# Kernel tuning notes

Measured on AMD Instinct MI355X. Metric: run time of the kernel, lower is better.

## Reference

```python
import jax, jax.numpy as jnp
import numpy as np
from jax import lax

D, NTOK, HEADS, DH, DEPTH, KCODE = 512, 256, 16, 32, 12, 2048

def _ln(x, g, b):
    m = x.mean(-1, keepdims=True)
    v = x.var(-1, keepdims=True)
    return (x - m) / jnp.sqrt(v + 1e-5) * g + b

def _attn(x, g, bln, wqkv, wo, bo):
    b, n, _ = x.shape
    xn = _ln(x, g, bln)
    qkv = xn @ wqkv  # [b,n,3*H*DH]
    q, k, v = jnp.split(qkv, 3, axis=-1)
    def h(t):
        return t.reshape(b, n, HEADS, DH).transpose(0, 2, 1, 3)  # bhnd
    q, k, v = h(q), h(k), h(v)
    dots = jnp.einsum('bhid,bhjd->bhij', q, k) * (DH ** -0.5)
    a = jax.nn.softmax(dots, axis=-1)
    o = jnp.einsum('bhij,bhjd->bhid', a, v).transpose(0, 2, 1, 3).reshape(b, n, HEADS * DH)
    return x + o @ wo + bo

def _conv3(x, w):  # w [out,in,3,3], pad 1
    return lax.conv_general_dilated(x, w, (1, 1), [(1, 1), (1, 1)],
                                    dimension_numbers=('NCHW', 'OIHW', 'NCHW'))

def _convT2(x, w, b):  # torch ConvTranspose2d k=2,s=2; w torch-shape [in,out,2,2]
    wk = jnp.transpose(w, (1, 0, 2, 3))[:, :, ::-1, ::-1]
    y = lax.conv_general_dilated(x, wk, (1, 1), [(1, 1), (1, 1)], lhs_dilation=(2, 2),
                                 dimension_numbers=('NCHW', 'OIHW', 'NCHW'))
    return y + b[None, :, None, None]

def _bn_relu(x, g, b):  # training-mode BatchNorm2d (biased var) + ReLU
    m = x.mean((0, 2, 3), keepdims=True)
    v = x.var((0, 2, 3), keepdims=True)
    xn = (x - m) / jnp.sqrt(v + 1e-5)
    return jax.nn.relu(xn * g[None, :, None, None] + b[None, :, None, None])

def setup_inputs() -> dict:
    key = jax.random.key(0)
    ks = iter(jax.random.split(key, 64))
    r = lambda *s: jax.random.normal(next(ks), s, dtype=jnp.float32)
    w = lambda *s: 0.02 * jax.random.normal(next(ks), s, dtype=jnp.float32)
    inp = {
        'x': r(16, 512, 16, 16),
        'feat0': r(16, 64, 128, 128),
        'feat1': r(16, 128, 64, 64),
        'feat2': r(16, 256, 32, 32),
        'pos_emb': r(1, NTOK, D),
        'codebook': r(KCODE, D),
        'ln_g': jnp.ones((DEPTH, D)), 'ln_b': jnp.zeros((DEPTH, D)),
        'wqkv': w(DEPTH, D, 3 * HEADS * DH),
        'wo': w(DEPTH, HEADS * DH, D), 'bo': jnp.zeros((DEPTH, D)),
        'up_w0': w(512, 256, 2, 2), 'up_b0': jnp.zeros((256,)),
        'cw0a': w(256, 512, 3, 3), 'g0a': jnp.ones((256,)), 'b0a': jnp.zeros((256,)),
        'cw0b': w(256, 256, 3, 3), 'g0b': jnp.ones((256,)), 'b0b': jnp.zeros((256,)),
        'up_w1': w(256, 128, 2, 2), 'up_b1': jnp.zeros((128,)),
        'cw1a': w(128, 256, 3, 3), 'g1a': jnp.ones((128,)), 'b1a': jnp.zeros((128,)),
        'cw1b': w(128, 128, 3, 3), 'g1b': jnp.ones((128,)), 'b1b': jnp.zeros((128,)),
        'up_w2': w(128, 64, 2, 2), 'up_b2': jnp.zeros((64,)),
        'cw2a': w(64, 128, 3, 3), 'g2a': jnp.ones((64,)), 'b2a': jnp.zeros((64,)),
        'cw2b': w(64, 64, 3, 3), 'g2b': jnp.ones((64,)), 'b2b': jnp.zeros((64,)),
        'last_w': w(1, 64, 1, 1), 'last_b': jnp.zeros((1,)),
    }
    return inp

def reference(x, feat0, feat1, feat2, pos_emb, codebook, ln_g, ln_b, wqkv, wo, bo,
              up_w0, up_b0, cw0a, g0a, b0a, cw0b, g0b, b0b,
              up_w1, up_b1, cw1a, g1a, b1a, cw1b, g1b, b1b,
              up_w2, up_b2, cw2a, g2a, b2a, cw2b, g2b, b2b,
              last_w, last_b):
    b = x.shape[0]
    # ViT encoder: flatten spatial -> tokens, add pos embedding, 12 residual attn layers
    tok = x.reshape(b, D, NTOK).transpose(0, 2, 1) + pos_emb  # [b,256,512]
    for i in range(DEPTH):
        tok = _attn(tok, ln_g[i], ln_b[i], wqkv[i], wo[i], bo[i])
    # VQ codebook quantization: squared-euclidean argmin + gather + straight-through
    flat = tok.reshape(-1, D)
    d2 = (flat * flat).sum(-1, keepdims=True) - 2.0 * flat @ codebook.T + (codebook * codebook).sum(-1)
    idx = jnp.argmin(d2, axis=-1)
    q = codebook[idx].reshape(b, NTOK, D)
    quant = tok + lax.stop_gradient(q - tok)
    y = quant.transpose(0, 2, 1).reshape(b, D, 16, 16)
    # conv decoder with skip connections (DecoderCup blocks)
    y = _convT2(y, up_w0, up_b0)                      # [b,256,32,32]
    y = jnp.concatenate([y, feat2], axis=1)           # [b,512,32,32]
    y = _bn_relu(_conv3(y, cw0a), g0a, b0a)
    y = _bn_relu(_conv3(y, cw0b), g0b, b0b)
    y = _convT2(y, up_w1, up_b1)                      # [b,128,64,64]
    y = jnp.concatenate([y, feat1], axis=1)
    y = _bn_relu(_conv3(y, cw1a), g1a, b1a)
    y = _bn_relu(_conv3(y, cw1b), g1b, b1b)
    y = _convT2(y, up_w2, up_b2)                      # [b,64,128,128]
    y = jnp.concatenate([y, feat0], axis=1)
    y = _bn_relu(_conv3(y, cw2a), g2a, b2a)
    y = _bn_relu(_conv3(y, cw2b), g2b, b2b)
    y = lax.conv_general_dilated(y, last_w, (1, 1), [(0, 0), (0, 0)],
                                 dimension_numbers=('NCHW', 'OIHW', 'NCHW')) + last_b[None, :, None, None]
    return jax.nn.sigmoid(y)  # [b,1,128,128]
```

## Files before the change

kernel.cpp:

```cpp
#include <hip/hip_runtime.h>

#define B_    16
#define NTOK  256
#define D_    512
#define HEADS 16
#define DH    32
#define DEPTH 12
#define KCODE 2048
#define M_    (B_*NTOK)
#define BN_S  512

typedef __attribute__((ext_vector_type(8))) short short8;
typedef __attribute__((ext_vector_type(4))) float float4v;
typedef __attribute__((ext_vector_type(16))) float float16v;
typedef __attribute__((ext_vector_type(4))) unsigned int uint4v;
typedef __attribute__((ext_vector_type(2))) unsigned int uint2v;
typedef unsigned short ushort;

__device__ __forceinline__ ushort f2b(float f){
  union { float f; unsigned u; } v; v.f = f;
  unsigned r = v.u + 0x7FFFu + ((v.u >> 16) & 1u);
  return (ushort)(r >> 16);
}
__device__ __forceinline__ float b2f(ushort h){
  union { unsigned u; float f; } v; v.u = ((unsigned)h) << 16; return v.f;
}
__device__ __forceinline__ float bits2f(unsigned u){
  union { unsigned u; float f; } v; v.u = u; return v.f;
}

typedef __attribute__((address_space(3))) unsigned int lds_uint;
typedef __attribute__((address_space(1))) const unsigned int glob_uint;
__device__ __forceinline__ void gl_lds16(const ushort* g, ushort* l){
  __builtin_amdgcn_global_load_lds((glob_uint*)g, (lds_uint*)l, 16, 0, 0);
}


__global__ void k_tok_init(const float* __restrict__ x, const float* __restrict__ pos,
                           float* __restrict__ tok){
  __shared__ float t[32][33];
  const int t0 = blockIdx.x*32, d0 = blockIdx.y*32, b = blockIdx.z;
  const int tx = threadIdx.x, ty = threadIdx.y;
  #pragma unroll
  for (int i = 0; i < 4; ++i){
    int d = d0 + ty + i*8;
    t[ty + i*8][tx] = x[((size_t)(b*D_ + d))*NTOK + t0 + tx];
  }
  __syncthreads();
  #pragma unroll
  for (int i = 0; i < 4; ++i){
    int tt = t0 + ty + i*8;
    tok[((size_t)(b*NTOK + tt))*D_ + d0 + tx] = t[tx][ty + i*8] + pos[(size_t)tt*D_ + d0 + tx];
  }
}

__global__ void k_split(const float* __restrict__ src, ushort* __restrict__ oh,
                        ushort* __restrict__ ol, int n){
  int i = blockIdx.x*256 + threadIdx.x;
  if (i >= n) return;
  float v = src[i];
  ushort h = f2b(v);
  oh[i] = h; ol[i] = f2b(v - b2f(h));
}

__global__ void k_split_t(const float* __restrict__ src, ushort* __restrict__ oh,
                          ushort* __restrict__ ol, int K, int N){
  __shared__ float t[32][33];
  const int n0 = blockIdx.x*32, k0 = blockIdx.y*32;
  const size_t lb = (size_t)blockIdx.z*K*N;
  const int tx = threadIdx.x, ty = threadIdx.y;
  #pragma unroll
  for (int i = 0; i < 4; ++i){
    int k = k0 + ty + i*8;
    t[ty + i*8][tx] = src[lb + (size_t)k*N + n0 + tx];
  }
  __syncthreads();
  #pragma unroll
  for (int i = 0; i < 4; ++i){
    int n = n0 + ty + i*8;
    float v = t[tx][ty + i*8];
    ushort h = f2b(v);
    size_t o = lb + (size_t)n*K + k0 + tx;
    oh[o] = h; ol[o] = f2b(v - b2f(h));
  }
}

__global__ void k_w9(const float* __restrict__ w, ushort* __restrict__ W9,
                     int Cin, int Cout){
  int i = blockIdx.x*256 + threadIdx.x;
  if (i >= Cout*Cin*9) return;
  int co = i / (Cin*9); int r = i - co*(Cin*9);
  int ci = r / 9; int tap = r - ci*9;
  W9[((size_t)tap*Cout + co)*Cin + ci] = f2b(w[i]);
}

__global__ void k_upw(const float* __restrict__ w, ushort* __restrict__ Wt4,
                      int Cin, int Cout){
  int i = blockIdx.x*256 + threadIdx.x;
  if (i >= Cin*Cout*4) return;
  int ci = i / (Cout*4); int r = i - ci*(Cout*4);
  int co = r >> 2; int tap = r & 3;
  Wt4[((size_t)tap*Cout + co)*Cin + ci] = f2b(w[i]);
}

__global__ __launch_bounds__(256) void k_ln_split(
    const float* __restrict__ in, ushort* __restrict__ oh,
    ushort* __restrict__ ol, const float* __restrict__ g,
    const float* __restrict__ bta){
  const int lane = threadIdx.x & 63;
  const int row  = blockIdx.x*4 + (threadIdx.x >> 6);
  const float* xr = in + (size_t)row*D_ + lane*8;
  float4v v0 = *(const float4v*)xr;
  float4v v1 = *(const float4v*)(xr + 4);
  float s = v0.x+v0.y+v0.z+v0.w + v1.x+v1.y+v1.z+v1.w;
  float q = v0.x*v0.x+v0.y*v0.y+v0.z*v0.z+v0.w*v0.w
          + v1.x*v1.x+v1.y*v1.y+v1.z*v1.z+v1.w*v1.w;
  #pragma unroll
  for (int off = 32; off > 0; off >>= 1){
    s += __shfl_xor(s, off, 64);
    q += __shfl_xor(q, off, 64);
  }
  float mean = s * (1.f/D_);
  float var  = q * (1.f/D_) - mean*mean;
  float inv  = rsqrtf(var + 1e-5f);
  float4v g0 = *(const float4v*)(g + lane*8);
  float4v g1 = *(const float4v*)(g + lane*8 + 4);
  float4v b0 = *(const float4v*)(bta + lane*8);
  float4v b1 = *(const float4v*)(bta + lane*8 + 4);
  float xv[8] = {v0.x,v0.y,v0.z,v0.w,v1.x,v1.y,v1.z,v1.w};
  float gv[8] = {g0.x,g0.y,g0.z,g0.w,g1.x,g1.y,g1.z,g1.w};
  float bv[8] = {b0.x,b0.y,b0.z,b0.w,b1.x,b1.y,b1.z,b1.w};
  unsigned hw[4], lw[4];
  #pragma unroll
  for (int p = 0; p < 4; ++p){
    float ya = (xv[2*p]   - mean)*inv*gv[2*p]   + bv[2*p];
    float yb = (xv[2*p+1] - mean)*inv*gv[2*p+1] + bv[2*p+1];
    ushort ha = f2b(ya), hb = f2b(yb);
    hw[p] = (unsigned)ha | ((unsigned)hb << 16);
    lw[p] = (unsigned)f2b(ya - b2f(ha)) | ((unsigned)f2b(yb - b2f(hb)) << 16);
  }
  size_t o = (size_t)row*D_ + lane*8;
  *(uint4v*)(oh + o) = uint4v{hw[0], hw[1], hw[2], hw[3]};
  *(uint4v*)(ol + o) = uint4v{lw[0], lw[1], lw[2], lw[3]};
}

__global__ __launch_bounds__(256,2) void k_gemm_split(
    const ushort* __restrict__ Ah, const ushort* __restrict__ Al,
    const ushort* __restrict__ Bh, const ushort* __restrict__ Bl,
    float* __restrict__ C, const float* __restrict__ bias,
    const float* __restrict__ resid, int M, int N, int K){
  __shared__ ushort Ash[128][32], Asl[128][32], Bsh[128][32], Bsl[128][32];
  const int tid = threadIdx.x;
  const int m_base = blockIdx.x*128, n_base = blockIdx.y*128;
  const int lane = tid & 63, wv = tid >> 6;
  const int quad = lane >> 4, r16 = lane & 15;
  const int m_off = (wv & 1)*64, n_off = (wv >> 1)*64;
  const int lrow = lane >> 2, lseg = lane & 3;
  const int row0 = wv*32 + lrow;
  const int us   = lseg ^ ((row0 >> 1) & 3);
  const size_t offA0 = (size_t)(m_base + row0)*K + us*8;
  const size_t offA1 = offA0 + (size_t)16*K;
  const size_t offB0 = (size_t)(n_base + row0)*K + us*8;
  const size_t offB1 = offB0 + (size_t)16*K;
  ushort* lAh = &Ash[0][0] + wv*1024;
  ushort* lAl = &Asl[0][0] + wv*1024;
  ushort* lBh = &Bsh[0][0] + wv*1024;
  ushort* lBl = &Bsl[0][0] + wv*1024;
  float4v acc[4][4];
  #pragma unroll
  for (int i = 0; i < 4; ++i)
    #pragma unroll
    for (int j = 0; j < 4; ++j) acc[i][j] = float4v{0.f,0.f,0.f,0.f};
  for (int k0 = 0; k0 < K; k0 += 32){
    gl_lds16(Ah + offA0 + k0, lAh);
    gl_lds16(Ah + offA1 + k0, lAh + 512);
    gl_lds16(Al + offA0 + k0, lAl);
    gl_lds16(Al + offA1 + k0, lAl + 512);
    gl_lds16(Bh + offB0 + k0, lBh);
    gl_lds16(Bh + offB1 + k0, lBh + 512);
    gl_lds16(Bl + offB0 + k0, lBl);
    gl_lds16(Bl + offB1 + k0, lBl + 512);
    __syncthreads();
    short8 ah[4], al[4], bh[4], bl[4];
    #pragma unroll
    for (int i = 0; i < 4; ++i){
      int ra = m_off + i*16 + r16;
      int rb = n_off + i*16 + r16;
      int sa = (quad ^ ((ra >> 1) & 3))*8;
      int sb = (quad ^ ((rb >> 1) & 3))*8;
      ah[i] = *(const short8*)&Ash[ra][sa];
      al[i] = *(const short8*)&Asl[ra][sa];
      bh[i] = *(const short8*)&Bsh[rb][sb];
      bl[i] = *(const short8*)&Bsl[rb][sb];
    }
    #pragma unroll
    for (int i = 0; i < 4; ++i)
      #pragma unroll
      for (int j = 0; j < 4; ++j){
        acc[i][j] = __builtin_amdgcn_mfma_f32_16x16x32_bf16(bh[j], ah[i], acc[i][j], 0,0,0);
        acc[i][j] = __builtin_amdgcn_mfma_f32_16x16x32_bf16(bh[j], al[i], acc[i][j], 0,0,0);
        acc[i][j] = __builtin_amdgcn_mfma_f32_16x16x32_bf16(bl[j], ah[i], acc[i][j], 0,0,0);
      }
    __syncthreads();
  }
  #pragma unroll
  for (int i = 0; i < 4; ++i){
    int m = m_base + m_off + i*16 + r16;
    #pragma unroll
    for (int j = 0; j < 4; ++j){
      int n = n_base + n_off + j*16 + quad*4;
      float4v v = acc[i][j];
      if (bias)  v += *(const float4v*)(bias + n);
      if (resid) v += *(const float4v*)(resid + (size_t)m*N + n);
      *(float4v*)(C + (size_t)m*N + n) = v;
    }
  }
}

__global__ __launch_bounds__(512) void k_attn2(const float* __restrict__ qkv,
                                               ushort* __restrict__ oh,
                                               ushort* __restrict__ ol){
  __shared__ float4v smem[NTOK*16];
  float4v* ks = smem;
  float4v* vs = smem + NTOK*8;
  const int h = blockIdx.x, b = blockIdx.y, t = threadIdx.x;
  const int tq = t & 255, half = t >> 8;
  const float* base = qkv + (size_t)b*NTOK*1536;
  const int koff = 512 + h*DH, voff = 1024 + h*DH;
  for (int i = t; i < NTOK*8; i += 512){
    int j = i >> 3, d4 = i & 7;
    ks[i] = *(const float4v*)(base + (size_t)j*1536 + koff + d4*4);
    vs[i] = *(const float4v*)(base + (size_t)j*1536 + voff + d4*4);
  }
  float4v q8[8];
  const float* qrow = base + (size_t)tq*1536 + h*DH;
  #pragma unroll
  for (int d4 = 0; d4 < 8; ++d4) q8[d4] = *(const float4v*)(qrow + d4*4);
  __syncthreads();
  float4v o8[8];
  #pragma unroll
  for (int d4 = 0; d4 < 8; ++d4) o8[d4] = float4v{0.f,0.f,0.f,0.f};
  float l = 0.f;
  const int j0 = half*128, j1 = j0 + 128;
  for (int j = j0; j < j1; ++j){
    float s = 0.f;
    #pragma unroll
    for (int d4 = 0; d4 < 8; ++d4){
      float4v kk = ks[j*8 + d4];
      s += q8[d4].x*kk.x + q8[d4].y*kk.y + q8[d4].z*kk.z + q8[d4].w*kk.w;
    }
    float e = __expf(s * 0.17677669529663689f);
    l += e;
    #pragma unroll
    for (int d4 = 0; d4 < 8; ++d4){
      float4v vv = vs[j*8 + d4];
      o8[d4].x += e*vv.x; o8[d4].y += e*vv.y; o8[d4].z += e*vv.z; o8[d4].w += e*vv.w;
    }
  }
  __syncthreads();
  if (half){
    float4v* st = smem + (size_t)tq*9;
    #pragma unroll
    for (int d4 = 0; d4 < 8; ++d4) st[d4] = o8[d4];
    ((float*)smem)[9216 + tq] = l;
  }
  __syncthreads();
  if (!half){
    const float4v* st = smem + (size_t)tq*9;
    #pragma unroll
    for (int d4 = 0; d4 < 8; ++d4) o8[d4] += st[d4];
    l += ((float*)smem)[9216 + tq];
    float inv = 1.f / l;
    size_t ob = (size_t)(b*NTOK + tq)*D_ + h*DH;
    #pragma unroll
    for (int d4 = 0; d4 < 8; ++d4){
      float vals[4] = {o8[d4].x*inv, o8[d4].y*inv, o8[d4].z*inv, o8[d4].w*inv};
      #pragma unroll
      for (int r = 0; r < 4; ++r){
        ushort hh = f2b(vals[r]);
        oh[ob + d4*4 + r] = hh;
        ol[ob + d4*4 + r] = f2b(vals[r] - b2f(hh));
      }
    }
  }
}

__global__ void k_cnorm(const float* __restrict__ cb, float* __restrict__ cnorm){
  int k = blockIdx.x, t = threadIdx.x;
  float v1 = cb[(size_t)k*D_ + t];
  float v2 = cb[(size_t)k*D_ + t + 256];
  __shared__ float r[256];
  r[t] = v1*v1 + v2*v2;
  __syncthreads();
  for (int off=128; off>0; off>>=1){
    if (t<off) r[t]+=r[t+off];
    __syncthreads();
  }
  if (t==0) cnorm[k] = r[0];
}

__global__ void k_argmin(const float* __restrict__ d2, const float* __restrict__ cnorm,
                         int* __restrict__ idx){
  int m = blockIdx.x, t = threadIdx.x;
  float best = 3.4e38f; int bk = 0;
  for (int k = t; k < KCODE; k += 256){
    float s = cnorm[k] - 2.f*d2[(size_t)m*KCODE + k];
    if (s < best){ best = s; bk = k; }
  }
  __shared__ float bs[256]; __shared__ int bi[256];
  bs[t]=best; bi[t]=bk;
  __syncthreads();
  for (int off=128; off>0; off>>=1){
    if (t<off){
      if (bs[t+off] < bs[t] || (bs[t+off]==bs[t] && bi[t+off]<bi[t])){
        bs[t]=bs[t+off]; bi[t]=bi[t+off];
      }
    }
    __syncthreads();
  }
  if (t==0) idx[m] = bi[0];
}

__global__ void k_gather_nhwc(const float* __restrict__ cb, const int* __restrict__ idx,
                              ushort* __restrict__ y0){
  int i = blockIdx.x*256 + threadIdx.x;
  if (i >= B_*NTOK*D_) return;
  int d = i % D_; int r = i / D_; int t = r % NTOK; int b = r / NTOK;
  y0[i] = f2b(cb[(size_t)idx[b*NTOK + t]*D_ + d]);
}


__global__ __launch_bounds__(256,2) void k_conv16(
    const ushort* __restrict__ X, const ushort* __restrict__ W9,
    float* __restrict__ Y, int Cin, int Cout, int H, int W){
  __shared__ ushort Xs[324][34];
  __shared__ ushort Ws[576][34];
  const int HW = H*W;
  const int tid = threadIdx.x;
  const int b = blockIdx.z;
  const int tiles_w = W >> 4;
  const int th0 = (blockIdx.x / tiles_w) * 16;
  const int tw0 = (blockIdx.x - (blockIdx.x / tiles_w)*tiles_w) * 16;
  const int n_base = blockIdx.y*64;
  const int lane = tid & 63, wv = tid >> 6;
  const int l31 = lane & 31, hi8 = (lane >> 5)*8;
  const ushort* Xb = X + (size_t)b*HW*Cin;
  const ushort* sptr[6]; ushort* sdst[6]; bool sok[6];
  #pragma unroll
  for (int e = 0; e < 6; ++e){
    int item = tid + e*256;
    int row = item >> 2;
    int seg = item & 3;
    if (row > 323) row = 323;
    int ph = row / 18, pw = row - ph*18;
    int gh = th0 + ph - 1, gw = tw0 + pw - 1;
    bool ok = gh >= 0 && gh < H && gw >= 0 && gw < W;
    int pidx = ok ? (gh*W + gw) : 0;
    sok[e] = ok;
    sptr[e] = Xb + ((size_t)pidx*Cin + seg*8);
    sdst[e] = &Xs[row][seg*8];
  }
  const ushort* wptr[9]; ushort* wdst[9];
  #pragma unroll
  for (int e = 0; e < 9; ++e){
    int item = tid + e*256;
    int row = item >> 2;
    int seg = item & 3;
    int tap = row >> 6, co = row & 63;
    wdst[e] = &Ws[row][seg*8];
    wptr[e] = W9 + ((size_t)tap*Cout + n_base + co)*Cin + seg*8;
  }
  const uint4v zz = {};
  float16v a00={}, a01={}, a10={}, a11={};
  const int lrow = (lane & 15) + ((lane & 16) ? 18 : 0);
  const int pr0 = wv*72 + lrow;
  for (int k0 = 0; k0 < Cin; k0 += 32){
    if (k0) __syncthreads();
    #pragma unroll
    for (int e = 0; e < 6; ++e){
      if (e < 5 || tid < 16){
        uint4v v = sok[e] ? *(const uint4v*)(sptr[e] + k0) : zz;
        *(uint4v*)sdst[e] = v;
      }
    }
    #pragma unroll
    for (int e = 0; e < 9; ++e)
      *(uint4v*)wdst[e] = *(const uint4v*)(wptr[e] + k0);
    __syncthreads();
    #pragma unroll
    for (int s = 0; s < 2; ++s){
      const int kc = s*16 + hi8;
      #pragma unroll
      for (int tap = 0; tap < 9; ++tap){
        const int kh = tap/3, kw = tap - (tap/3)*3;
        const int xr = pr0 + kh*18 + kw;
        short8 x0 = *(const short8*)&Xs[xr     ][kc];
        short8 x1 = *(const short8*)&Xs[xr + 36][kc];
        short8 w0 = *(const short8*)&Ws[tap*64      + l31][kc];
        short8 w1 = *(const short8*)&Ws[tap*64 + 32 + l31][kc];
        a00 = __builtin_amdgcn_mfma_f32_32x32x16_bf16(w0, x0, a00, 0,0,0);
        a01 = __builtin_amdgcn_mfma_f32_32x32x16_bf16(w0, x1, a01, 0,0,0);
        a10 = __builtin_amdgcn_mfma_f32_32x32x16_bf16(w1, x0, a10, 0,0,0);
        a11 = __builtin_amdgcn_mfma_f32_32x32x16_bf16(w1, x1, a11, 0,0,0);
      }
    }
  }
  float* Yb = Y + (size_t)b*HW*Cout;
  const int co4 = (lane >> 5)*4;
  #pragma unroll
  for (int i = 0; i < 2; ++i){
    int p = wv*64 + i*32 + l31;
    int gp = (th0 + (p >> 4))*W + tw0 + (p & 15);
    float* yr = Yb + (size_t)gp*Cout + n_base + co4;
    float16v A0 = i ? a01 : a00;
    float16v A1 = i ? a11 : a10;
    #pragma unroll
    for (int q = 0; q < 4; ++q){
      float4v v0 = {A0[4*q+0], A0[4*q+1], A0[4*q+2], A0[4*q+3]};
      float4v v1 = {A1[4*q+0], A1[4*q+1], A1[4*q+2], A1[4*q+3]};
      *(float4v*)(yr + 8*q)      = v0;
      *(float4v*)(yr + 32 + 8*q) = v1;
    }
  }
}

__global__ __launch_bounds__(256) void k_upconv_nhwc(
    const ushort* __restrict__ X, const ushort* __restrict__ Wt4,
    const float* __restrict__ bias, ushort* __restrict__ CC,
    int Cin, int Cout, int Hi, int Wi, int Ctot){
  __shared__ ushort Xs[64][40], Ws[4][64][40];
  const int HWi = Hi*Wi;
  const int tid = threadIdx.x;
  const int b = blockIdx.z;
  const int m_base = blockIdx.x*64;
  const int n_base = blockIdx.y*64;
  const int lane = tid & 63, wv = tid >> 6;
  const int quad = lane >> 4, r16 = lane & 15;
  const int m_off = (wv & 1)*32, n_off = (wv >> 1)*32;
  const int srow = tid & 63, skq = tid >> 6;
  const ushort* xrow = X + ((size_t)b*HWi + m_base + srow)*Cin + skq*8;
  const ushort* w0 = Wt4 + ((size_t)0*Cout + n_base + srow)*Cin + skq*8;
  const ushort* w1 = Wt4 + ((size_t)1*Cout + n_base + srow)*Cin + skq*8;
  const ushort* w2 = Wt4 + ((size_t)2*Cout + n_base + srow)*Cin + skq*8;
  const ushort* w3 = Wt4 + ((size_t)3*Cout + n_base + srow)*Cin + skq*8;
  float4v acc[4][4];
  #pragma unroll
  for (int t = 0; t < 4; ++t)
    #pragma unroll
    for (int q = 0; q < 4; ++q) acc[t][q] = float4v{0.f,0.f,0.f,0.f};
  for (int k0 = 0; k0 < Cin; k0 += 32){
    *(uint4v*)&Xs[srow][skq*8]    = *(const uint4v*)(xrow + k0);
    *(uint4v*)&Ws[0][srow][skq*8] = *(const uint4v*)(w0 + k0);
    *(uint4v*)&Ws[1][srow][skq*8] = *(const uint4v*)(w1 + k0);
    *(uint4v*)&Ws[2][srow][skq*8] = *(const uint4v*)(w2 + k0);
    *(uint4v*)&Ws[3][srow][skq*8] = *(const uint4v*)(w3 + k0);
    __syncthreads();
    short8 xf0 = *(const short8*)&Xs[m_off      + r16][quad*8];
    short8 xf1 = *(const short8*)&Xs[m_off + 16 + r16][quad*8];
    #pragma unroll
    for (int t = 0; t < 4; ++t){
      short8 wf0 = *(const short8*)&Ws[t][n_off      + r16][quad*8];
      short8 wf1 = *(const short8*)&Ws[t][n_off + 16 + r16][quad*8];
      acc[t][0] = __builtin_amdgcn_mfma_f32_16x16x32_bf16(wf0, xf0, acc[t][0], 0,0,0);
      acc[t][1] = __builtin_amdgcn_mfma_f32_16x16x32_bf16(wf0, xf1, acc[t][1], 0,0,0);
      acc[t][2] = __builtin_amdgcn_mfma_f32_16x16x32_bf16(wf1, xf0, acc[t][2], 0,0,0);
      acc[t][3] = __builtin_amdgcn_mfma_f32_16x16x32_bf16(wf1, xf1, acc[t][3], 0,0,0);
    }
    __syncthreads();
  }
  const int Wo = 2*Wi, HWo = 4*HWi;
  int co0 = n_base + n_off + quad*4, co1 = co0 + 16;
  float4v bv0 = *(const float4v*)(bias + co0);
  float4v bv1 = *(const float4v*)(bias + co1);
  int px0 = m_base + m_off + r16, px1 = px0 + 16;
  #pragma unroll
  for (int j = 0; j < 2; ++j){
    int p = j ? px1 : px0;
    int r = p / Wi, c = p - r*Wi;
    #pragma unroll
    for (int t = 0; t < 4; ++t){
      int opix = (2*r + (t>>1))*Wo + 2*c + (t&1);
      ushort* o = CC + ((size_t)b*HWo + opix)*Ctot;
      float4v vA = acc[t][0 + j] + bv0;
      float4v vB = acc[t][2 + j] + bv1;
      uint2v pA, pB;
      pA.x = (unsigned)f2b(vA.x) | ((unsigned)f2b(vA.y) << 16);
      pA.y = (unsigned)f2b(vA.z) | ((unsigned)f2b(vA.w) << 16);
      pB.x = (unsigned)f2b(vB.x) | ((unsigned)f2b(vB.y) << 16);
      pB.y = (unsigned)f2b(vB.z) | ((unsigned)f2b(vB.w) << 16);
      *(uint2v*)(o + co0) = pA;
      *(uint2v*)(o + co1) = pB;
    }
  }
}

__global__ void k_feat2cc(const float* __restrict__ feat, ushort* __restrict__ cc,
                          int Cf, int Coff, int Ctot, int HW){
  __shared__ ushort t[32][33];
  int pb = blockIdx.x*32, cbs = blockIdx.y*32, b = blockIdx.z;
  int tx = threadIdx.x, ty = threadIdx.y;
  #pragma unroll
  for (int i = 0; i < 4; ++i){
    int c = cbs + ty + i*8;
    t[ty + i*8][tx] = f2b(feat[((size_t)(b*Cf) + c)*HW + pb + tx]);
  }
  __syncthreads();
  #pragma unroll
  for (int i = 0; i < 4; ++i){
    int p = pb + ty + i*8;
    cc[((size_t)b*HW + p)*Ctot + Coff + cbs + tx] = t[tx][ty + i*8];
  }
}

__global__ __launch_bounds__(256) void k_bnstats_nhwc(
    const float* __restrict__ x, float* __restrict__ part, int C, int HW){
  const int s = blockIdx.x, tid = threadIdx.x;
  const int R = B_*HW;
  const int chunk = R / BN_S;
  const int L = C >> 2;
  const int G = 256 / L;
  const int c4 = tid % L, g = tid / L;
  float4v a = {}, q = {};
  const float* xb = x + (size_t)(s*chunk)*C + 4*c4;
  for (int r = g; r < chunk; r += G){
    float4v v = *(const float4v*)(xb + (size_t)r*C);
    a += v; q += v*v;
  }
  __shared__ float4v h1[256], h2[256];
  h1[tid] = a; h2[tid] = q;
  __syncthreads();
  if (tid < L){
    float4v ra = h1[tid], rq = h2[tid];
    for (int gg = 1; gg < G; ++gg){ ra += h1[tid + gg*L]; rq += h2[tid + gg*L]; }
    int c0 = 4*c4;
    part[(size_t)(c0+0)*BN_S + s] = ra.x;
    part[(size_t)(c0+1)*BN_S + s] = ra.y;
    part[(size_t)(c0+2)*BN_S + s] = ra.z;
    part[(size_t)(c0+3)*BN_S + s] = ra.w;
    part[(size_t)(C+c0+0)*BN_S + s] = rq.x;
    part[(size_t)(C+c0+1)*BN_S + s] = rq.y;
    part[(size_t)(C+c0+2)*BN_S + s] = rq.z;
    part[(size_t)(C+c0+3)*BN_S + s] = rq.w;
  }
}

__global__ void k_bnfinal(const float* __restrict__ part, const float* __restrict__ g,
                          const float* __restrict__ bb, float* __restrict__ scale,
                          float* __restrict__ shift, int C, int cnt){
  int c = blockIdx.x, t = threadIdx.x;
  __shared__ float r1[256], r2[256];
  r1[t] = part[(size_t)c*BN_S + t]       + part[(size_t)c*BN_S + t + 256];
  r2[t] = part[(size_t)(C + c)*BN_S + t] + part[(size_t)(C + c)*BN_S + t + 256];
  __syncthreads();
  for (int off = 128; off > 0; off >>= 1){
    if (t < off){ r1[t] += r1[t+off]; r2[t] += r2[t+off]; }
    __syncthreads();
  }
  if (t == 0){
    float m = r1[0]/cnt;
    float v = r2[0]/cnt - m*m;
    float sc = g[c]*rsqrtf(v + 1e-5f);
    scale[c] = sc;
    shift[c] = bb[c] - m*sc;
  }
}

__global__ void k_bnapply_nhwc(const float* __restrict__ x, ushort* __restrict__ y,
                               const float* __restrict__ scale,
                               const float* __restrict__ shift, int C, int n4){
  int i = blockIdx.x*256 + threadIdx.x;
  if (i >= n4) return;
  float4v v = *(const float4v*)(x + (size_t)4*i);
  int c0 = (4*i) % C;
  float4v sc = *(const float4v*)(scale + c0);
  float4v sh = *(const float4v*)(shift + c0);
  float r0 = fmaxf(v.x*sc.x + sh.x, 0.f);
  float r1 = fmaxf(v.y*sc.y + sh.y, 0.f);
  float r2 = fmaxf(v.z*sc.z + sh.z, 0.f);
  float r3 = fmaxf(v.w*sc.w + sh.w, 0.f);
  uint2v pk;
  pk.x = (unsigned)f2b(r0) | ((unsigned)f2b(r1) << 16);
  pk.y = (unsigned)f2b(r2) | ((unsigned)f2b(r3) << 16);
  *(uint2v*)(y + (size_t)4*i) = pk;
}

__global__ void k_last_nhwc(const ushort* __restrict__ x, const float* __restrict__ lw,
                            const float* __restrict__ lb, float* __restrict__ out){
  __shared__ float wsm[64];
  int tid = threadIdx.x;
  if (tid < 64) wsm[tid] = lw[tid];
  __syncthreads();
  int i = blockIdx.x*256 + tid;
  const uint4v* xr = (const uint4v*)(x + (size_t)i*64);
  float acc = lb[0];
  #pragma unroll
  for (int q = 0; q < 8; ++q){
    uint4v u = xr[q];
    unsigned uu[4] = {u.x, u.y, u.z, u.w};
    #pragma unroll
    for (int k = 0; k < 4; ++k){
      acc += bits2f(uu[k] << 16)          * wsm[q*8 + 2*k];
      acc += bits2f(uu[k] & 0xffff0000u)  * wsm[q*8 + 2*k + 1];
    }
  }
  out[i] = 1.f/(1.f + __expf(-acc));
}

#define MBx 1048576ull

static inline void run_conv16(const ushort* in, const float* w, ushort* W9,
                              float* out, int Cin, int Cout, int H, int W,
                              hipStream_t stream){
  int total = Cout*Cin*9;
  k_w9<<<(total+255)/256, 256, 0, stream>>>(w, W9, Cin, Cout);
  k_conv16<<<dim3((H>>4)*(W>>4), Cout/64, B_), 256, 0, stream>>>(in, W9, out, Cin, Cout, H, W);
}

static inline void run_bn(const float* x, ushort* y, float* part, float* scale, float* shift,
                          const float* g, const float* bb, int C, int HW, hipStream_t stream){
  k_bnstats_nhwc<<<BN_S, 256, 0, stream>>>(x, part, C, HW);
  k_bnfinal<<<C, 256, 0, stream>>>(part, g, bb, scale, shift, C, B_*HW);
  int n4 = B_*HW*C/4;
  k_bnapply_nhwc<<<(n4+255)/256, 256, 0, stream>>>(x, y, scale, shift, C, n4);
}

extern "C" void kernel_launch(void* const* d_in, const int* in_sizes, int n_in,
                              void* d_out, int out_size, void* d_ws, size_t ws_size,
                              hipStream_t stream){
  const float* x     = (const float*)d_in[0];
  const float* feat0 = (const float*)d_in[1];
  const float* feat1 = (const float*)d_in[2];
  const float* feat2 = (const float*)d_in[3];
  const float* pos   = (const float*)d_in[4];
  const float* cb    = (const float*)d_in[5];
  const float* ln_g  = (const float*)d_in[6];
  const float* ln_b  = (const float*)d_in[7];
  const float* wqkv  = (const float*)d_in[8];
  const float* wo    = (const float*)d_in[9];
  const float* bo    = (const float*)d_in[10];
  const float* up_w0 = (const float*)d_in[11];
  const float* up_b0 = (const float*)d_in[12];
  const float* cw0a  = (const float*)d_in[13];
  const float* g0a   = (const float*)d_in[14];
  const float* b0a   = (const float*)d_in[15];
  const float* cw0b  = (const float*)d_in[16];
  const float* g0b   = (const float*)d_in[17];
  const float* b0b   = (const float*)d_in[18];
  const float* up_w1 = (const float*)d_in[19];
  const float* up_b1 = (const float*)d_in[20];
  const float* cw1a  = (const float*)d_in[21];
  const float* g1a   = (const float*)d_in[22];
  const float* b1a   = (const float*)d_in[23];
  const float* cw1b  = (const float*)d_in[24];
  const float* g1b   = (const float*)d_in[25];
  const float* b1b   = (const float*)d_in[26];
  const float* up_w2 = (const float*)d_in[27];
  const float* up_b2 = (const float*)d_in[28];
  const float* cw2a  = (const float*)d_in[29];
  const float* g2a   = (const float*)d_in[30];
  const float* b2a   = (const float*)d_in[31];
  const float* cw2b  = (const float*)d_in[32];
  const float* g2b   = (const float*)d_in[33];
  const float* b2b   = (const float*)d_in[34];
  const float* lw    = (const float*)d_in[35];
  const float* lb    = (const float*)d_in[36];

  char* ws = (char*)d_ws;
  float*  tok     = (float*) (ws);
  ushort* xn_hi   = (ushort*)(ws +  8388608ull);
  ushort* xn_lo   = (ushort*)(ws + 12582912ull);
  float*  qkv     = (float*) (ws + 16777216ull);
  ushort* at_hi   = (ushort*)(ws + 41943040ull);
  ushort* at_lo   = (ushort*)(ws + 46137344ull);
  ushort* tok_hi  = (ushort*)(ws + 50331648ull);
  ushort* tok_lo  = (ushort*)(ws + 54525952ull);
  ushort* Wq_hi   = (ushort*)(ws + 58720256ull);
  ushort* Wq_lo   = (ushort*)(ws + 77594624ull);
  ushort* Wo_hi   = (ushort*)(ws + 96468992ull);
  ushort* Wo_lo   = (ushort*)(ws + 102760448ull);
  ushort* cb_hi   = (ushort*)(ws + 109051904ull);
  ushort* cb_lo   = (ushort*)(ws + 111149056ull);
  float*  cnorm   = (float*) (ws + 113246208ull);
  int*    idx     = (int*)   (ws + 113254400ull);
  float*  d2      = (float*) (ws + 58720256ull);
  ushort* W9   = (ushort*)(ws + 134*MBx);
  float* bnsc  = (float*) (ws + 136*MBx + 524288);
  float* bnsh  = (float*) (ws + 136*MBx + 528384);
  ushort* Wt4  = (ushort*)(ws + 137*MBx);
  float* bnp   = (float*) (ws + 138*MBx);
  ushort* y0   = (ushort*)(ws + 139*MBx);
  ushort* cc0 = (ushort*)(ws + 146*MBx);
  float*  va0 = (float*) (ws + 163*MBx);
  ushort* xa0 = (ushort*)(ws + 180*MBx);
  float*  vb0 = (float*) (ws + 146*MBx);
  ushort* xb0 = (ushort*)(ws + 189*MBx);
  ushort* cc1 = (ushort*)(ws + 0*MBx);
  float*  va1 = (float*) (ws + 34*MBx);
  ushort* xa1 = (ushort*)(ws + 68*MBx);
  float*  vb1 = (float*) (ws + 85*MBx);
  ushort* xb1 = (ushort*)(ws + 146*MBx);
  ushort* cc2 = (ushort*)(ws + 0*MBx);
  float*  va2 = (float*) (ws + 67*MBx);
  ushort* xa2 = (ushort*)(ws + 146*MBx);
  float*  vb2 = (float*) (ws + 0*MBx);
  ushort* xb2 = (ushort*)(ws + 67*MBx);

  k_split_t<<<dim3(1536/32, D_/32, DEPTH), dim3(32,8), 0, stream>>>(wqkv, Wq_hi, Wq_lo, D_, 1536);
  k_split_t<<<dim3(D_/32, D_/32, DEPTH), dim3(32,8), 0, stream>>>(wo, Wo_hi, Wo_lo, D_, D_);
  k_split<<<(KCODE*D_+255)/256, 256, 0, stream>>>(cb, cb_hi, cb_lo, KCODE*D_);
  k_cnorm<<<KCODE, 256, 0, stream>>>(cb, cnorm);

  k_tok_init<<<dim3(NTOK/32, D_/32, B_), dim3(32,8), 0, stream>>>(x, pos, tok);
  for (int l = 0; l < DEPTH; ++l){
    k_ln_split<<<M_/4, 256, 0, stream>>>(tok, xn_hi, xn_lo, ln_g + l*D_, ln_b + l*D_);
    k_gemm_split<<<dim3(M_/128, 1536/128), 256, 0, stream>>>(
        xn_hi, xn_lo, Wq_hi + (size_t)l*1536*D_, Wq_lo + (size_t)l*1536*D_,
        qkv, nullptr, nullptr, M_, 1536, D_);
    k_attn2<<<dim3(HEADS, B_), 512, 0, stream>>>(qkv, at_hi, at_lo);
    k_gemm_split<<<dim3(M_/128, D_/128), 256, 0, stream>>>(
        at_hi, at_lo, Wo_hi + (size_t)l*D_*D_, Wo_lo + (size_t)l*D_*D_,
        tok, bo + l*D_, tok, M_, D_, D_);
  }

  k_split<<<(M_*D_+255)/256, 256, 0, stream>>>(tok, tok_hi, tok_lo, M_*D_);
  k_gemm_split<<<dim3(M_/128, KCODE/128), 256, 0, stream>>>(
      tok_hi, tok_lo, cb_hi, cb_lo, d2, nullptr, nullptr, M_, KCODE, D_);
  k_argmin<<<M_, 256, 0, stream>>>(d2, cnorm, idx);
  k_gather_nhwc<<<(B_*NTOK*D_)/256, 256, 0, stream>>>(cb, idx, y0);

  k_upw<<<(512*256*4+255)/256, 256, 0, stream>>>(up_w0, Wt4, 512, 256);
  k_upconv_nhwc<<<dim3(256/64, 256/64, B_), 256, 0, stream>>>(y0, Wt4, up_b0, cc0, 512, 256, 16, 16, 512);
  k_feat2cc<<<dim3(1024/32, 256/32, B_), dim3(32,8), 0, stream>>>(feat2, cc0, 256, 256, 512, 1024);
  run_conv16(cc0, cw0a, W9, va0, 512, 256, 32, 32, stream);
  run_bn(va0, xa0, bnp, bnsc, bnsh, g0a, b0a, 256, 1024, stream);
  run_conv16(xa0, cw0b, W9, vb0, 256, 256, 32, 32, stream);
  run_bn(vb0, xb0, bnp, bnsc, bnsh, g0b, b0b, 256, 1024, stream);

  k_upw<<<(256*128*4+255)/256, 256, 0, stream>>>(up_w1, Wt4, 256, 128);
  k_upconv_nhwc<<<dim3(1024/64, 128/64, B_), 256, 0, stream>>>(xb0, Wt4, up_b1, cc1, 256, 128, 32, 32, 256);
  k_feat2cc<<<dim3(4096/32, 128/32, B_), dim3(32,8), 0, stream>>>(feat1, cc1, 128, 128, 256, 4096);
  run_conv16(cc1, cw1a, W9, va1, 256, 128, 64, 64, stream);
  run_bn(va1, xa1, bnp, bnsc, bnsh, g1a, b1a, 128, 4096, stream);
  run_conv16(xa1, cw1b, W9, vb1, 128, 128, 64, 64, stream);
  run_bn(vb1, xb1, bnp, bnsc, bnsh, g1b, b1b, 128, 4096, stream);

  k_upw<<<(128*64*4+255)/256, 256, 0, stream>>>(up_w2, Wt4, 128, 64);
  k_upconv_nhwc<<<dim3(4096/64, 64/64, B_), 256, 0, stream>>>(xb1, Wt4, up_b2, cc2, 128, 64, 64, 64, 128);
  k_feat2cc<<<dim3(16384/32, 64/32, B_), dim3(32,8), 0, stream>>>(feat0, cc2, 64, 64, 128, 16384);
  run_conv16(cc2, cw2a, W9, va2, 128, 64, 128, 128, stream);
  run_bn(va2, xa2, bnp, bnsc, bnsh, g2a, b2a, 64, 16384, stream);
  run_conv16(xa2, cw2b, W9, vb2, 64, 64, 128, 128, stream);
  run_bn(vb2, xb2, bnp, bnsc, bnsh, g2b, b2b, 64, 16384, stream);

  k_last_nhwc<<<(B_*16384)/256, 256, 0, stream>>>(xb2, lw, lb, (float*)d_out);
}
```

Before: 2.172 ms.

## Split-K the 32x32 decoder convs and coalesce weight-repack kernels

The first decoder stage's two 3x3 convs (32x32 spatial, 4 tiles per image) now split the input-channel reduction in two. This doubles the block count to fill more compute units, and each half writes its own fp32 partial buffer. The BN stats and apply kernels take an optional second buffer and sum the partials on the fly, so no separate reduction kernel is needed. The w9 and upconv weight repack kernels are rewritten for coalesced reads (9 contiguous taps per thread) and an LDS transpose. The cost is extra fp32 partial traffic, and workspace buffers are remapped, which risks aliasing.

```diff
diff --git a/kernel.cpp b/kernel.cpp
--- a/kernel.cpp
+++ b/kernel.cpp
@@ -88,19 +88,36 @@
 __global__ void k_w9(const float* __restrict__ w, ushort* __restrict__ W9,
                      int Cin, int Cout){
   int i = blockIdx.x*256 + threadIdx.x;
-  if (i >= Cout*Cin*9) return;
-  int co = i / (Cin*9); int r = i - co*(Cin*9);
-  int ci = r / 9; int tap = r - ci*9;
-  W9[((size_t)tap*Cout + co)*Cin + ci] = f2b(w[i]);
+  if (i >= Cout*Cin) return;
+  const float* src = w + (size_t)i*9;
+  float v[9];
+  #pragma unroll
+  for (int t = 0; t < 9; ++t) v[t] = src[t];
+  const size_t CC = (size_t)Cout*Cin;
+  #pragma unroll
+  for (int t = 0; t < 9; ++t) W9[t*CC + i] = f2b(v[t]);
 }
 
 __global__ void k_upw(const float* __restrict__ w, ushort* __restrict__ Wt4,
                       int Cin, int Cout){
-  int i = blockIdx.x*256 + threadIdx.x;
-  if (i >= Cin*Cout*4) return;
-  int ci = i / (Cout*4); int r = i - ci*(Cout*4);
-  int co = r >> 2; int tap = r & 3;
-  Wt4[((size_t)tap*Cout + co)*Cin + ci] = f2b(w[i]);
+  __shared__ ushort t4[4][32][33];
+  const int co0 = blockIdx.x*32, ci0 = blockIdx.y*32;
+  const int tx = threadIdx.x, ty = threadIdx.y;
+  #pragma unroll
+  for (int i = 0; i < 4; ++i){
+    int ci = ty + i*8;
+    float4v v = *(const float4v*)(w + ((size_t)(ci0+ci)*Cout + co0+tx)*4);
+    t4[0][tx][ci] = f2b(v.x); t4[1][tx][ci] = f2b(v.y);
+    t4[2][tx][ci] = f2b(v.z); t4[3][tx][ci] = f2b(v.w);
+  }
+  __syncthreads();
+  #pragma unroll
+  for (int i = 0; i < 4; ++i){
+    int co = ty + i*8;
+    #pragma unroll
+    for (int tap = 0; tap < 4; ++tap)
+      Wt4[((size_t)tap*Cout + co0+co)*Cin + ci0 + tx] = t4[tap][co][tx];
+  }
 }
 
 __global__ __launch_bounds__(256) void k_ln_split(
@@ -332,12 +349,15 @@
 
 __global__ __launch_bounds__(256,2) void k_conv16(
     const ushort* __restrict__ X, const ushort* __restrict__ W9,
-    float* __restrict__ Y, int Cin, int Cout, int H, int W){
+    float* __restrict__ Y, int Cin, int Cout, int H, int W, int ksplit){
   __shared__ ushort Xs[324][34];
   __shared__ ushort Ws[576][34];
   const int HW = H*W;
   const int tid = threadIdx.x;
-  const int b = blockIdx.z;
+  const int b = blockIdx.z % B_;
+  const int split = blockIdx.z / B_;
+  const int CinS = Cin / ksplit;
+  const int kbeg = split*CinS, kend = kbeg + CinS;
   const int tiles_w = W >> 4;
   const int th0 = (blockIdx.x / tiles_w) * 16;
   const int tw0 = (blockIdx.x - (blockIdx.x / tiles_w)*tiles_w) * 16;
@@ -374,8 +394,8 @@
   float16v a00={}, a01={}, a10={}, a11={};
   const int lrow = (lane & 15) + ((lane & 16) ? 18 : 0);
   const int pr0 = wv*72 + lrow;
-  for (int k0 = 0; k0 < Cin; k0 += 32){
-    if (k0) __syncthreads();
+  for (int k0 = kbeg; k0 < kend; k0 += 32){
+    if (k0 != kbeg) __syncthreads();
     #pragma unroll
     for (int e = 0; e < 6; ++e){
       if (e < 5 || tid < 16){
@@ -405,7 +425,7 @@
       }
     }
   }
-  float* Yb = Y + (size_t)b*HW*Cout;
+  float* Yb = Y + ((size_t)split*B_ + b)*HW*Cout;
   const int co4 = (lane >> 5)*4;
   #pragma unroll
   for (int i = 0; i < 2; ++i){
@@ -513,7 +533,8 @@
 }
 
 __global__ __launch_bounds__(256) void k_bnstats_nhwc(
-    const float* __restrict__ x, float* __restrict__ part, int C, int HW){
+    const float* __restrict__ x, const float* __restrict__ x2,
+    float* __restrict__ part, int C, int HW){
   const int s = blockIdx.x, tid = threadIdx.x;
   const int R = B_*HW;
   const int chunk = R / BN_S;
@@ -521,9 +542,12 @@
   const int G = 256 / L;
   const int c4 = tid % L, g = tid / L;
   float4v a = {}, q = {};
-  const float* xb = x + (size_t)(s*chunk)*C + 4*c4;
+  const size_t base = (size_t)(s*chunk)*C + 4*c4;
+  const float* xb = x + base;
+  const float* xb2 = x2 ? x2 + base : nullptr;
   for (int r = g; r < chunk; r += G){
     float4v v = *(const float4v*)(xb + (size_t)r*C);
+    if (xb2) v += *(const float4v*)(xb2 + (size_t)r*C);
     a += v; q += v*v;
   }
   __shared__ float4v h1[256], h2[256];
@@ -565,12 +589,14 @@
   }
 }
 
-__global__ void k_bnapply_nhwc(const float* __restrict__ x, ushort* __restrict__ y,
+__global__ void k_bnapply_nhwc(const float* __restrict__ x, const float* __restrict__ x2,
+                               ushort* __restrict__ y,
                                const float* __restrict__ scale,
                                const float* __restrict__ shift, int C, int n4){
   int i = blockIdx.x*256 + threadIdx.x;
   if (i >= n4) return;
   float4v v = *(const float4v*)(x + (size_t)4*i);
+  if (x2) v += *(const float4v*)(x2 + (size_t)4*i);
   int c0 = (4*i) % C;
   float4v sc = *(const float4v*)(scale + c0);
   float4v sh = *(const float4v*)(shift + c0);
@@ -610,18 +636,19 @@
 
 static inline void run_conv16(const ushort* in, const float* w, ushort* W9,
                               float* out, int Cin, int Cout, int H, int W,
-                              hipStream_t stream){
-  int total = Cout*Cin*9;
+                              int ks, hipStream_t stream){
+  int total = Cout*Cin;
   k_w9<<<(total+255)/256, 256, 0, stream>>>(w, W9, Cin, Cout);
-  k_conv16<<<dim3((H>>4)*(W>>4), Cout/64, B_), 256, 0, stream>>>(in, W9, out, Cin, Cout, H, W);
-}
-
-static inline void run_bn(const float* x, ushort* y, float* part, float* scale, float* shift,
+  k_conv16<<<dim3((H>>4)*(W>>4), Cout/64, B_*ks), 256, 0, stream>>>(in, W9, out, Cin, Cout, H, W, ks);
+}
+
+static inline void run_bn(const float* x, const float* x2, ushort* y, float* part,
+                          float* scale, float* shift,
                           const float* g, const float* bb, int C, int HW, hipStream_t stream){
-  k_bnstats_nhwc<<<BN_S, 256, 0, stream>>>(x, part, C, HW);
+  k_bnstats_nhwc<<<BN_S, 256, 0, stream>>>(x, x2, part, C, HW);
   k_bnfinal<<<C, 256, 0, stream>>>(part, g, bb, scale, shift, C, B_*HW);
   int n4 = B_*HW*C/4;
-  k_bnapply_nhwc<<<(n4+255)/256, 256, 0, stream>>>(x, y, scale, shift, C, n4);
+  k_bnapply_nhwc<<<(n4+255)/256, 256, 0, stream>>>(x, x2, y, scale, shift, C, n4);
 }
 
 extern "C" void kernel_launch(void* const* d_in, const int* in_sizes, int n_in,
@@ -689,11 +716,11 @@
   ushort* Wt4  = (ushort*)(ws + 137*MBx);
   float* bnp   = (float*) (ws + 138*MBx);
   ushort* y0   = (ushort*)(ws + 139*MBx);
-  ushort* cc0 = (ushort*)(ws + 146*MBx);
-  float*  va0 = (float*) (ws + 163*MBx);
-  ushort* xa0 = (ushort*)(ws + 180*MBx);
-  float*  vb0 = (float*) (ws + 146*MBx);
-  ushort* xb0 = (ushort*)(ws + 189*MBx);
+  ushort* cc0  = (ushort*)(ws + 146*MBx);
+  float*  va0s = (float*) (ws + 34*MBx);
+  ushort* xa0  = (ushort*)(ws + 180*MBx);
+  float*  vb0s = (float*) (ws + 0*MBx);
+  ushort* xb0  = (ushort*)(ws + 189*MBx);
   ushort* cc1 = (ushort*)(ws + 0*MBx);
   float*  va1 = (float*) (ws + 34*MBx);
   ushort* xa1 = (ushort*)(ws + 68*MBx);
@@ -728,29 +755,29 @@
   k_argmin<<<M_, 256, 0, stream>>>(d2, cnorm, idx);
   k_gather_nhwc<<<(B_*NTOK*D_)/256, 256, 0, stream>>>(cb, idx, y0);
 
-  k_upw<<<(512*256*4+255)/256, 256, 0, stream>>>(up_w0, Wt4, 512, 256);
+  k_upw<<<dim3(256/32, 512/32), dim3(32,8), 0, stream>>>(up_w0, Wt4, 512, 256);
   k_upconv_nhwc<<<dim3(256/64, 256/64, B_), 256, 0, stream>>>(y0, Wt4, up_b0, cc0, 512, 256, 16, 16, 512);
   k_feat2cc<<<dim3(1024/32, 256/32, B_), dim3(32,8), 0, stream>>>(feat2, cc0, 256, 256, 512, 1024);
-  run_conv16(cc0, cw0a, W9, va0, 512, 256, 32, 32, stream);
-  run_bn(va0, xa0, bnp, bnsc, bnsh, g0a, b0a, 256, 1024, stream);
-  run_conv16(xa0, cw0b, W9, vb0, 256, 256, 32, 32, stream);
-  run_bn(vb0, xb0, bnp, bnsc, bnsh, g0b, b0b, 256, 1024, stream);
-
-  k_upw<<<(256*128*4+255)/256, 256, 0, stream>>>(up_w1, Wt4, 256, 128);
+  run_conv16(cc0, cw0a, W9, va0s, 512, 256, 32, 32, 2, stream);
+  run_bn(va0s, va0s + (size_t)B_*1024*256, xa0, bnp, bnsc, bnsh, g0a, b0a, 256, 1024, stream);
+  run_conv16(xa0, cw0b, W9, vb0s, 256, 256, 32, 32, 2, stream);
+  run_bn(vb0s, vb0s + (size_t)B_*1024*256, xb0, bnp, bnsc, bnsh, g0b, b0b, 256, 1024, stream);
+
+  k_upw<<<dim3(128/32, 256/32), dim3(32,8), 0, stream>>>(up_w1, Wt4, 256, 128);
   k_upconv_nhwc<<<dim3(1024/64, 128/64, B_), 256, 0, stream>>>(xb0, Wt4, up_b1, cc1, 256, 128, 32, 32, 256);
   k_feat2cc<<<dim3(4096/32, 128/32, B_), dim3(32,8), 0, stream>>>(feat1, cc1, 128, 128, 256, 4096);
-  run_conv16(cc1, cw1a, W9, va1, 256, 128, 64, 64, stream);
-  run_bn(va1, xa1, bnp, bnsc, bnsh, g1a, b1a, 128, 4096, stream);
-  run_conv16(xa1, cw1b, W9, vb1, 128, 128, 64, 64, stream);
-  run_bn(vb1, xb1, bnp, bnsc, bnsh, g1b, b1b, 128, 4096, stream);
-
-  k_upw<<<(128*64*4+255)/256, 256, 0, stream>>>(up_w2, Wt4, 128, 64);
+  run_conv16(cc1, cw1a, W9, va1, 256, 128, 64, 64, 1, stream);
+  run_bn(va1, nullptr, xa1, bnp, bnsc, bnsh, g1a, b1a, 128, 4096, stream);
+  run_conv16(xa1, cw1b, W9, vb1, 128, 128, 64, 64, 1, stream);
+  run_bn(vb1, nullptr, xb1, bnp, bnsc, bnsh, g1b, b1b, 128, 4096, stream);
+
+  k_upw<<<dim3(64/32, 128/32), dim3(32,8), 0, stream>>>(up_w2, Wt4, 128, 64);
   k_upconv_nhwc<<<dim3(4096/64, 64/64, B_), 256, 0, stream>>>(xb1, Wt4, up_b2, cc2, 128, 64, 64, 64, 128);
   k_feat2cc<<<dim3(16384/32, 64/32, B_), dim3(32,8), 0, stream>>>(feat0, cc2, 64, 64, 128, 16384);
-  run_conv16(cc2, cw2a, W9, va2, 128, 64, 128, 128, stream);
-  run_bn(va2, xa2, bnp, bnsc, bnsh, g2a, b2a, 64, 16384, stream);
-  run_conv16(xa2, cw2b, W9, vb2, 64, 64, 128, 128, stream);
-  run_bn(vb2, xb2, bnp, bnsc, bnsh, g2b, b2b, 64, 16384, stream);
+  run_conv16(cc2, cw2a, W9, va2, 128, 64, 128, 128, 1, stream);
+  run_bn(va2, nullptr, xa2, bnp, bnsc, bnsh, g2a, b2a, 64, 16384, stream);
+  run_conv16(xa2, cw2b, W9, vb2, 64, 64, 128, 128, 1, stream);
+  run_bn(vb2, nullptr, xb2, bnp, bnsc, bnsh, g2b, b2b, 64, 16384, stream);
 
   k_last_nhwc<<<(B_*16384)/256, 256, 0, stream>>>(xb2, lw, lb, (float*)d_out);
 }
```

After: 2.149 ms. About the same (-1.0%).
